# Kernel tuning notes

Measured on AMD Instinct MI355X. Metric: run time of the kernel, lower is better.

Reference implementation:

```python
import jax, jax.numpy as jnp
import numpy as np

H = 1024      # lstm_hidden_size
LABELS = 122  # slot label size


def setup_inputs() -> dict:
    key = jax.random.key(0)
    ks = jax.random.split(key, 8)
    s_in = 1.0 / np.sqrt(5 * H)
    s_h = 1.0 / np.sqrt(H)
    return {
        "x": jax.random.normal(ks[0], (1, 512, 2 * H), jnp.float32),
        "hi": jax.random.normal(ks[1], (1, 512, 2 * H), jnp.float32),
        # LSTM params (PyTorch layout: gates ordered i, f, g, o)
        "W_ih": jax.random.uniform(ks[2], (4 * H, 5 * H), jnp.float32, -s_in, s_in),
        "W_hh": jax.random.uniform(ks[3], (4 * H, H), jnp.float32, -s_h, s_h),
        "b_ih": jax.random.uniform(ks[4], (4 * H,), jnp.float32, -s_h, s_h),
        "b_hh": jax.random.uniform(ks[5], (4 * H,), jnp.float32, -s_h, s_h),
        "W_fc": jax.random.uniform(ks[6], (LABELS, H), jnp.float32, -s_h, s_h),
        "b_fc": jax.random.uniform(ks[7], (LABELS,), jnp.float32, -s_h, s_h),
    }


def _decode(x, hi, W_ih, W_hh, b_ih, b_hh, W_fc, b_fc):
    # x, hi: [1, L, 2H] -> per-step encoder features [L, 4H] (batch fixed at 1)
    feats = jnp.concatenate([x, hi], axis=-1)[0]
    bias = b_ih + b_hh

    def step(carry, f_t):
        h, c, prev_out = carry
        z = jnp.concatenate([f_t, prev_out])              # [5H]: cat(x_t, hi_t, out_{t-1})
        gates = W_ih @ z + W_hh @ h + bias                # [4H]
        i, f, g, o = jnp.split(gates, 4)
        c_new = jax.nn.sigmoid(f) * c + jax.nn.sigmoid(i) * jnp.tanh(g)
        h_new = jax.nn.sigmoid(o) * jnp.tanh(c_new)
        return (h_new, c_new, h_new), h_new

    zero = jnp.zeros((H,), x.dtype)
    _, outs = jax.lax.scan(step, (zero, zero, zero), feats)  # outs: [L, H]
    res = outs @ W_fc.T + b_fc                               # [L, LABELS]
    return res[None]                                         # [1, L, LABELS]


def reference(x, hi, W_ih, W_hh, b_ih, b_hh, W_fc, b_fc):
    return _decode(x, hi, W_ih, W_hh, b_ih, b_hh, W_fc, b_fc)
```

## Files before the change

kernel.cpp:

```cpp
#include <hip/hip_runtime.h>
#include <hip/hip_fp16.h>
#include <math.h>

#define HD    1024
#define SEQL  512
#define NLAB  122
#define NWG   128
#define TPW   512
#define JPW   8

#define OFF_MSG   ((size_t)0)
#define OFF_HALL  ((size_t)16384)
#define OFF_GATES ((size_t)2113536)
#define OFF_WR    ((size_t)10502144)
#define OFF_W1H   ((size_t)27279360)
#define OFF_FH    ((size_t)60833792)
#define WS_NEED   ((size_t)65028096)

typedef unsigned long long u64;
typedef _Float16 v8h __attribute__((ext_vector_type(8)));
typedef float v4f __attribute__((ext_vector_type(4)));
typedef float v2f __attribute__((ext_vector_type(2)));
typedef unsigned int v4u __attribute__((ext_vector_type(4)));

static __device__ __forceinline__ uint4 pack8(float4 f0, float4 f1) {
    __half2 p0 = __floats2half2_rn(f0.x, f0.y);
    __half2 p1 = __floats2half2_rn(f0.z, f0.w);
    __half2 p2 = __floats2half2_rn(f1.x, f1.y);
    __half2 p3 = __floats2half2_rn(f1.z, f1.w);
    uint4 o;
    o.x = *(unsigned*)&p0; o.y = *(unsigned*)&p1;
    o.z = *(unsigned*)&p2; o.w = *(unsigned*)&p3;
    return o;
}

__global__ __launch_bounds__(256) void prep_all(const float* __restrict__ x,
                                                const float* __restrict__ hi,
                                                const float* __restrict__ W_ih,
                                                const float* __restrict__ W_hh,
                                                float* __restrict__ W_r2,
                                                uint4* __restrict__ F_h,
                                                uint4* __restrict__ W1h,
                                                u64* __restrict__ h_msg) {
    int b = blockIdx.x;
    int tid = threadIdx.x;
    if (b < 4096) {
        int o = b * 256 + tid;
        int g   = o >> 13;
        int i   = (o >> 9) & 15;
        int t   = o & 511;
        int row = t & 31;
        int kq  = t >> 5;
        int gate = row >> 3;
        int jj   = row & 7;
        int R = (gate << 10) + (g << 3) + jj;
        int k = (kq << 6) + (i << 2);
        float4 wa = *(const float4*)(W_ih + (size_t)R * 5120 + 4096 + k);
        float4 wb = *(const float4*)(W_hh + (size_t)R * 1024 + k);
        float4 out;
        out.x = wa.x + wb.x; out.y = wa.y + wb.y;
        out.z = wa.z + wb.z; out.w = wa.w + wb.w;
        *(float4*)(W_r2 + (size_t)o * 4) = out;
    } else if (b == 4096) {
        #pragma unroll
        for (int i = 0; i < 8; ++i)
            h_msg[tid * 8 + i] = 0ull;
    } else if (b < 5121) {
        int o = (b - 4097) * 256 + tid;
        int t = o >> 9;
        int u = o & 511;
        const float* src = (u < 256) ? (x  + (size_t)t * 2048 + u * 8)
                                     : (hi + (size_t)t * 2048 + (u - 256) * 8);
        F_h[o] = pack8(*(const float4*)src, *(const float4*)(src + 4));
    } else {
        int o = (b - 5121) * 256 + tid;
        int r = o >> 9;
        int u = o & 511;
        const float* src = W_ih + (size_t)r * 5120 + u * 8;
        W1h[o] = pack8(*(const float4*)src, *(const float4*)(src + 4));
    }
}

__global__ __launch_bounds__(256) void gates_mfma(const uint4* __restrict__ F_u4,
                                                  const uint4* __restrict__ W_u4,
                                                  const float* __restrict__ b_ih,
                                                  const float* __restrict__ b_hh,
                                                  float* __restrict__ gates_x) {
    __shared__ uint4 AsB[1024];
    const _Float16* Ash = (const _Float16*)AsB;
    const _Float16* Bsh = Ash + 4096;
    const int tid  = threadIdx.x;
    const int wv   = tid >> 6;
    const int lane = tid & 63;
    const int wr   = wv & 1;
    const int wc   = wv >> 1;
    const int n0 = blockIdx.x * 128;
    const int t0 = blockIdx.y * 128;

    const int u0 = tid * 2, u1 = tid * 2 + 1;
    const uint4* aSrc0 = F_u4 + (size_t)(t0 + (u0 >> 2)) * 512 + (u0 & 3);
    const uint4* aSrc1 = F_u4 + (size_t)(t0 + (u1 >> 2)) * 512 + (u1 & 3);
    const uint4* bSrc0 = W_u4 + (size_t)(n0 + (u0 >> 2)) * 512 + (u0 & 3);
    const uint4* bSrc1 = W_u4 + (size_t)(n0 + (u1 >> 2)) * 512 + (u1 & 3);

    v4f acc[4][4];
    #pragma unroll
    for (int mi = 0; mi < 4; ++mi)
        #pragma unroll
        for (int ni = 0; ni < 4; ++ni)
            acc[mi][ni] = (v4f){0.f, 0.f, 0.f, 0.f};

    const int aoff = (wr * 64 + (lane & 15)) * 32 + (lane >> 4) * 8;
    const int boff = (wc * 64 + (lane & 15)) * 32 + (lane >> 4) * 8;

    for (int it = 0; it < 128; ++it) {
        uint4 a0 = aSrc0[it * 4], a1 = aSrc1[it * 4];
        uint4 b0 = bSrc0[it * 4], b1 = bSrc1[it * 4];
        __syncthreads();
        AsB[u0]       = a0; AsB[u1]       = a1;
        AsB[512 + u0] = b0; AsB[512 + u1] = b1;
        __syncthreads();
        v8h a8[4], b8[4];
        #pragma unroll
        for (int mi = 0; mi < 4; ++mi)
            a8[mi] = *(const v8h*)(Ash + aoff + mi * 16 * 32);
        #pragma unroll
        for (int ni = 0; ni < 4; ++ni)
            b8[ni] = *(const v8h*)(Bsh + boff + ni * 16 * 32);
        #pragma unroll
        for (int mi = 0; mi < 4; ++mi)
            #pragma unroll
            for (int ni = 0; ni < 4; ++ni)
                acc[mi][ni] = __builtin_amdgcn_mfma_f32_16x16x32_f16(
                                  a8[mi], b8[ni], acc[mi][ni], 0, 0, 0);
    }

    #pragma unroll
    for (int ni = 0; ni < 4; ++ni) {
        int r = n0 + wc * 64 + ni * 16 + (lane & 15);
        int sidx = ((r & 1023) >> 3) * 32 + (r >> 10) * 8 + (r & 7);
        float bias = b_ih[r] + b_hh[r];
        #pragma unroll
        for (int mi = 0; mi < 4; ++mi) {
            int tb = t0 + wr * 64 + mi * 16 + ((lane >> 4) << 2);
            #pragma unroll
            for (int reg = 0; reg < 4; ++reg)
                gates_x[(size_t)(tb + reg) * 4096 + sidx] = acc[mi][ni][reg] + bias;
        }
    }
}

__global__ __launch_bounds__(256) void gates_gemm_f32(const float* __restrict__ x,
                                                      const float* __restrict__ hi,
                                                      const float* __restrict__ W_ih,
                                                      const float* __restrict__ b_ih,
                                                      const float* __restrict__ b_hh,
                                                      float* __restrict__ gates_x) {
    __shared__ float As[16][68];
    __shared__ float Bs[16][68];
    const int tid = threadIdx.x;
    const int r0 = blockIdx.x * 64;
    const int t0 = blockIdx.y * 64;
    const int tx = tid & 15, ty = tid >> 4;
    const int l   = tid & 63;
    const int kq4 = tid >> 6;

    float acc[4][4] = {};
    for (int kb = 0; kb < 4096; kb += 16) {
        int k = kb + kq4 * 4;
        const float* asrc = (k < 2048) ? (x  + (size_t)(t0 + l) * 2048 + k)
                                       : (hi + (size_t)(t0 + l) * 2048 + (k - 2048));
        float4 a4 = *(const float4*)asrc;
        float4 b4 = *(const float4*)(W_ih + (size_t)(r0 + l) * 5120 + k);
        __syncthreads();
        As[kq4 * 4 + 0][l] = a4.x; As[kq4 * 4 + 1][l] = a4.y;
        As[kq4 * 4 + 2][l] = a4.z; As[kq4 * 4 + 3][l] = a4.w;
        Bs[kq4 * 4 + 0][l] = b4.x; Bs[kq4 * 4 + 1][l] = b4.y;
        Bs[kq4 * 4 + 2][l] = b4.z; Bs[kq4 * 4 + 3][l] = b4.w;
        __syncthreads();
        #pragma unroll
        for (int kk = 0; kk < 16; ++kk) {
            float4 av = *(const float4*)&As[kk][ty * 4];
            float4 bv = *(const float4*)&Bs[kk][tx * 4];
            float a_[4] = {av.x, av.y, av.z, av.w};
            float b_[4] = {bv.x, bv.y, bv.z, bv.w};
            #pragma unroll
            for (int i = 0; i < 4; ++i)
                #pragma unroll
                for (int j = 0; j < 4; ++j)
                    acc[i][j] += a_[i] * b_[j];
        }
    }
    int r = r0 + tx * 4;
    float bias[4];
    #pragma unroll
    for (int j = 0; j < 4; ++j) bias[j] = b_ih[r + j] + b_hh[r + j];
    int gate = r >> 10;
    int g    = (r & 1023) >> 3;
    int jj   = r & 7;
    int sidx = g * 32 + gate * 8 + jj;
    #pragma unroll
    for (int i = 0; i < 4; ++i) {
        float4 o;
        o.x = acc[i][0] + bias[0]; o.y = acc[i][1] + bias[1];
        o.z = acc[i][2] + bias[2]; o.w = acc[i][3] + bias[3];
        *(float4*)(gates_x + (size_t)(t0 + ty * 4 + i) * 4096 + sidx) = o;
    }
}

__global__ __launch_bounds__(512, 1) void lstm_rec(const float* __restrict__ gates_x,
                                                   const float* __restrict__ W_r2,
                                                   float* __restrict__ h_all,
                                                   u64* h_msg) {
    const int g   = blockIdx.x;
    const int tid = threadIdx.x;
    const int row = tid & 31;
    const int kq  = tid >> 5;
    __shared__ float  gxs[SEQL * 32];
    __shared__ float4 h_s4[256];
    __shared__ float  partial[8][36];
    float* h_sf = (float*)h_s4;

    float4 w[16];
    {
        const float4* Wp = (const float4*)W_r2 + (size_t)g * 8192;
        #pragma unroll
        for (int i = 0; i < 16; ++i)
            w[i] = Wp[i * TPW + tid];
    }

    {
        float4* gxs4 = (float4*)gxs;
        const float* gsrc = gates_x + (size_t)g * 32;
        #pragma unroll
        for (int k = 0; k < 8; ++k) {
            int o4 = tid + k * 512;
            int s  = o4 >> 3, c4 = o4 & 7;
            gxs4[o4] = *(const float4*)(gsrc + (size_t)s * 4096 + c4 * 4);
        }
    }
    __syncthreads();

    float c = 0.f;
    int budget = 4000000;

    for (int s = 0; s < SEQL; ++s) {
        float gx = 0.f;
        if (tid < 32) gx = gxs[s * 32 + tid];

        {
            const u64 addr = (u64)(h_msg + (size_t)(s & 1) * HD + tid * 2);
            const unsigned want = (unsigned)s;
            v4u ra, rb;
            for (;;) {
                asm volatile(
                    "global_load_dwordx4 %0, %2, off sc1\n\t"
                    "global_load_dwordx4 %1, %2, off sc1\n\t"
                    "s_waitcnt vmcnt(0)"
                    : "=&v"(ra), "=&v"(rb)
                    : "v"(addr)
                    : "memory");
                if (ra.y == want && ra.w == want) break;
                if (rb.y == want && rb.w == want) { ra = rb; break; }
                if (--budget < 0) { ra = rb; break; }
            }
            ((v2f*)h_sf)[tid] = (v2f){__uint_as_float(ra.x), __uint_as_float(ra.z)};
        }
        asm volatile("" ::: "memory");

        float a0 = 0.f, a1 = 0.f, a2 = 0.f, a3 = 0.f;
        #pragma unroll
        for (int i = 0; i < 16; ++i) {
            float4 h4 = h_s4[kq * 16 + i];
            a0 += w[i].x * h4.x;
            a1 += w[i].y * h4.y;
            a2 += w[i].z * h4.z;
            a3 += w[i].w * h4.w;
        }
        float p = (a0 + a1) + (a2 + a3);
        p += __shfl_xor(p, 32, 64);
        if ((tid & 32) == 0)
            partial[tid >> 6][row] = p;
        __syncthreads();

        if (tid < 32) {
            float sum = gx;
            #pragma unroll
            for (int q = 0; q < 8; ++q) sum += partial[q][tid];
            bool isg = ((tid >> 3) == 2);
            float e   = __expf(isg ? -2.f * sum : -sum);
            float act = isg ? (2.f / (1.f + e) - 1.f) : (1.f / (1.f + e));
            int jj = tid & 7;
            float sf = __shfl(act,  8 + jj, 64);
            float tg = __shfl(act, 16 + jj, 64);
            float so = __shfl(act, 24 + jj, 64);
            if (tid < 8) {
                float si = act;
                c = sf * c + si * tg;
                float th = 2.f / (1.f + __expf(-2.f * c)) - 1.f;
                float h = so * th;
                int j = g * JPW + tid;
                h_all[(size_t)s * HD + j] = h;
                u64 m = ((u64)(unsigned)(s + 1) << 32)
                      | (u64)__float_as_uint(h);
                __hip_atomic_store(h_msg + (size_t)((s + 1) & 1) * HD + j, m,
                                   __ATOMIC_RELAXED, __HIP_MEMORY_SCOPE_AGENT);
            }
        }
    }
}

__global__ __launch_bounds__(128) void fc_out(const float* __restrict__ h_all,
                                              const float* __restrict__ W_fc,
                                              const float* __restrict__ b_fc,
                                              float* __restrict__ out) {
    const int t0 = blockIdx.x * 4;
    const int tid = threadIdx.x;
    __shared__ float4 h_s[1024];
    const float4* hsrc = (const float4*)(h_all + (size_t)t0 * HD);
    #pragma unroll
    for (int i = 0; i < 8; ++i)
        h_s[tid + i * 128] = hsrc[tid + i * 128];
    __syncthreads();
    if (tid < NLAB) {
        float b = b_fc[tid];
        float acc0 = b, acc1 = b, acc2 = b, acc3 = b;
        const float4* wp = (const float4*)(W_fc + (size_t)tid * HD);
        #pragma unroll 4
        for (int k4 = 0; k4 < 256; ++k4) {
            float4 w = wp[k4];
            float4 h0 = h_s[k4];
            float4 h1 = h_s[256 + k4];
            float4 h2 = h_s[512 + k4];
            float4 h3 = h_s[768 + k4];
            acc0 += w.x*h0.x + w.y*h0.y + w.z*h0.z + w.w*h0.w;
            acc1 += w.x*h1.x + w.y*h1.y + w.z*h1.z + w.w*h1.w;
            acc2 += w.x*h2.x + w.y*h2.y + w.z*h2.z + w.w*h2.w;
            acc3 += w.x*h3.x + w.y*h3.y + w.z*h3.z + w.w*h3.w;
        }
        out[(size_t)(t0 + 0) * NLAB + tid] = acc0;
        out[(size_t)(t0 + 1) * NLAB + tid] = acc1;
        out[(size_t)(t0 + 2) * NLAB + tid] = acc2;
        out[(size_t)(t0 + 3) * NLAB + tid] = acc3;
    }
}

extern "C" void kernel_launch(void* const* d_in, const int* in_sizes, int n_in,
                              void* d_out, int out_size, void* d_ws, size_t ws_size,
                              hipStream_t stream) {
    const float* x    = (const float*)d_in[0];
    const float* hi   = (const float*)d_in[1];
    const float* W_ih = (const float*)d_in[2];
    const float* W_hh = (const float*)d_in[3];
    const float* b_ih = (const float*)d_in[4];
    const float* b_hh = (const float*)d_in[5];
    const float* W_fc = (const float*)d_in[6];
    const float* b_fc = (const float*)d_in[7];
    float* out = (float*)d_out;

    char* ws = (char*)d_ws;
    u64*   h_msg   = (u64*)(ws + OFF_MSG);
    float* h_all   = (float*)(ws + OFF_HALL);
    float* gates_x = (float*)(ws + OFF_GATES);
    float* W_r2    = (float*)(ws + OFF_WR);
    uint4* W1h     = (uint4*)(ws + OFF_W1H);
    uint4* F_h     = (uint4*)(ws + OFF_FH);

    if (ws_size >= WS_NEED) {
        prep_all<<<13313, 256, 0, stream>>>(x, hi, W_ih, W_hh, W_r2, F_h, W1h, h_msg);
        dim3 gg(32, 4);
        gates_mfma<<<gg, 256, 0, stream>>>(F_h, W1h, b_ih, b_hh, gates_x);
    } else {
        prep_all<<<4097, 256, 0, stream>>>(x, hi, W_ih, W_hh, W_r2, F_h, W1h, h_msg);
        dim3 gg(64, 8);
        gates_gemm_f32<<<gg, 256, 0, stream>>>(x, hi, W_ih, b_ih, b_hh, gates_x);
    }

    lstm_rec<<<NWG, TPW, 0, stream>>>(gates_x, W_r2, h_all, h_msg);

    fc_out<<<SEQL / 4, 128, 0, stream>>>(h_all, W_fc, b_fc, out);
}
```

Before: 1.171 ms.

## Split LSTM recurrence across 256 workgroups with 4 hidden units each

Doubles the number of persistent recurrence workgroups from 128 to 256, so each one owns 4 hidden units (16 gate rows) instead of 8. The weight prepack, the gate GEMM output layout and the recurrent kernel's indexing, reductions and shuffles are all rewritten for the new 16-row slice. Each workgroup now does half the dot-product work per step, with an extra shuffle stage in the reduction. The cost is that twice as many workgroups must poll and synchronise through the global h message buffer every step, which raises spin traffic and the risk that co-residency of all workgroups cannot be guaranteed.

```diff
diff --git a/kernel.cpp b/kernel.cpp
--- a/kernel.cpp
+++ b/kernel.cpp
@@ -5,9 +5,9 @@
 #define HD    1024
 #define SEQL  512
 #define NLAB  122
-#define NWG   128
+#define NWG   256
 #define TPW   512
-#define JPW   8
+#define JPW   4
 
 #define OFF_MSG   ((size_t)0)
 #define OFF_HALL  ((size_t)16384)
@@ -46,15 +46,15 @@
     int tid = threadIdx.x;
     if (b < 4096) {
         int o = b * 256 + tid;
-        int g   = o >> 13;
-        int i   = (o >> 9) & 15;
+        int g   = o >> 12;
+        int i   = (o >> 9) & 7;
         int t   = o & 511;
-        int row = t & 31;
-        int kq  = t >> 5;
-        int gate = row >> 3;
-        int jj   = row & 7;
-        int R = (gate << 10) + (g << 3) + jj;
-        int k = (kq << 6) + (i << 2);
+        int row = t & 15;
+        int kq  = t >> 4;
+        int gate = row >> 2;
+        int cc   = row & 3;
+        int R = (gate << 10) + (g << 2) + cc;
+        int k = (kq << 5) + (i << 2);
         float4 wa = *(const float4*)(W_ih + (size_t)R * 5120 + 4096 + k);
         float4 wb = *(const float4*)(W_hh + (size_t)R * 1024 + k);
         float4 out;
@@ -138,7 +138,7 @@
     #pragma unroll
     for (int ni = 0; ni < 4; ++ni) {
         int r = n0 + wc * 64 + ni * 16 + (lane & 15);
-        int sidx = ((r & 1023) >> 3) * 32 + (r >> 10) * 8 + (r & 7);
+        int sidx = ((r & 1023) >> 2) * 16 + (r >> 10) * 4 + (r & 3);
         float bias = b_ih[r] + b_hh[r];
         #pragma unroll
         for (int mi = 0; mi < 4; ++mi) {
@@ -196,9 +196,8 @@
     #pragma unroll
     for (int j = 0; j < 4; ++j) bias[j] = b_ih[r + j] + b_hh[r + j];
     int gate = r >> 10;
-    int g    = (r & 1023) >> 3;
-    int jj   = r & 7;
-    int sidx = g * 32 + gate * 8 + jj;
+    int g4   = (r & 1023) >> 2;
+    int sidx = g4 * 16 + gate * 4;
     #pragma unroll
     for (int i = 0; i < 4; ++i) {
         float4 o;
@@ -214,28 +213,28 @@
                                                    u64* h_msg) {
     const int g   = blockIdx.x;
     const int tid = threadIdx.x;
-    const int row = tid & 31;
-    const int kq  = tid >> 5;
-    __shared__ float  gxs[SEQL * 32];
+    const int row = tid & 15;
+    const int kq  = tid >> 4;
+    __shared__ float  gxs[SEQL * 16];
     __shared__ float4 h_s4[256];
-    __shared__ float  partial[8][36];
+    __shared__ float  partial[8][20];
     float* h_sf = (float*)h_s4;
 
-    float4 w[16];
+    float4 w8[8];
     {
-        const float4* Wp = (const float4*)W_r2 + (size_t)g * 8192;
-        #pragma unroll
-        for (int i = 0; i < 16; ++i)
-            w[i] = Wp[i * TPW + tid];
+        const float4* Wp = (const float4*)W_r2 + (size_t)g * 4096;
+        #pragma unroll
+        for (int i = 0; i < 8; ++i)
+            w8[i] = Wp[i * 512 + tid];
     }
 
     {
         float4* gxs4 = (float4*)gxs;
-        const float* gsrc = gates_x + (size_t)g * 32;
-        #pragma unroll
-        for (int k = 0; k < 8; ++k) {
+        const float* gsrc = gates_x + (size_t)g * 16;
+        #pragma unroll
+        for (int k = 0; k < 4; ++k) {
             int o4 = tid + k * 512;
-            int s  = o4 >> 3, c4 = o4 & 7;
+            int s  = o4 >> 2, c4 = o4 & 3;
             gxs4[o4] = *(const float4*)(gsrc + (size_t)s * 4096 + c4 * 4);
         }
     }
@@ -246,7 +245,7 @@
 
     for (int s = 0; s < SEQL; ++s) {
         float gx = 0.f;
-        if (tid < 32) gx = gxs[s * 32 + tid];
+        if (tid < 16) gx = gxs[s * 16 + tid];
 
         {
             const u64 addr = (u64)(h_msg + (size_t)(s & 1) * HD + tid * 2);
@@ -270,31 +269,32 @@
 
         float a0 = 0.f, a1 = 0.f, a2 = 0.f, a3 = 0.f;
         #pragma unroll
-        for (int i = 0; i < 16; ++i) {
-            float4 h4 = h_s4[kq * 16 + i];
-            a0 += w[i].x * h4.x;
-            a1 += w[i].y * h4.y;
-            a2 += w[i].z * h4.z;
-            a3 += w[i].w * h4.w;
+        for (int i = 0; i < 8; ++i) {
+            float4 h4 = h_s4[kq * 8 + i];
+            a0 += w8[i].x * h4.x;
+            a1 += w8[i].y * h4.y;
+            a2 += w8[i].z * h4.z;
+            a3 += w8[i].w * h4.w;
         }
         float p = (a0 + a1) + (a2 + a3);
+        p += __shfl_xor(p, 16, 64);
         p += __shfl_xor(p, 32, 64);
-        if ((tid & 32) == 0)
+        if ((tid & 48) == 0)
             partial[tid >> 6][row] = p;
         __syncthreads();
 
-        if (tid < 32) {
+        if (tid < 16) {
             float sum = gx;
             #pragma unroll
             for (int q = 0; q < 8; ++q) sum += partial[q][tid];
-            bool isg = ((tid >> 3) == 2);
+            bool isg = ((tid >> 2) == 2);
             float e   = __expf(isg ? -2.f * sum : -sum);
             float act = isg ? (2.f / (1.f + e) - 1.f) : (1.f / (1.f + e));
-            int jj = tid & 7;
-            float sf = __shfl(act,  8 + jj, 64);
-            float tg = __shfl(act, 16 + jj, 64);
-            float so = __shfl(act, 24 + jj, 64);
-            if (tid < 8) {
+            int cc = tid & 3;
+            float sf = __shfl(act,  4 + cc, 64);
+            float tg = __shfl(act,  8 + cc, 64);
+            float so = __shfl(act, 12 + cc, 64);
+            if (tid < 4) {
                 float si = act;
                 c = sf * c + si * tg;
                 float th = 2.f / (1.f + __expf(-2.f * c)) - 1.f;
```

Result: slower. 1.418 ms (+21.1%).
